# Kernel optimization log

Measured on AMD Instinct MI355X. Metric: run time of the kernel, lower is better.

The kernel has to match this reference:

```python
import jax, jax.numpy as jnp
import numpy as np

D = 768
H = 12
DH = 64
S = 1500
SCALE = 0.125  # 1/sqrt(64)


def setup_inputs() -> dict:
    key = jax.random.key(0)
    ks = jax.random.split(key, 8)
    def w(k):
        return jax.random.normal(k, (D, D), dtype=jnp.float32) * (1.0 / np.sqrt(D))
    x = jax.random.normal(ks[0], (8, S, D), dtype=jnp.float32)
    return {
        "x": x,
        "Wq": w(ks[1]), "bq": jax.random.normal(ks[2], (D,), dtype=jnp.float32) * 0.02,
        "Wk": w(ks[3]),
        "Wv": w(ks[4]), "bv": jax.random.normal(ks[5], (D,), dtype=jnp.float32) * 0.02,
        "Wo": w(ks[6]), "bo": jax.random.normal(ks[7], (D,), dtype=jnp.float32) * 0.02,
    }


def reference(x, Wq, bq, Wk, Wv, bv, Wo, bo):
    B = x.shape[0]
    # torch Linear: y = x @ W.T + b
    q = (jnp.einsum('bsd,ed->bse', x, Wq) + bq) * SCALE
    k = jnp.einsum('bsd,ed->bse', x, Wk)
    v = jnp.einsum('bsd,ed->bse', x, Wv) + bv
    # split heads: [B, S, H, DH] -> [B, H, S, DH]
    q = q.reshape(B, S, H, DH).transpose(0, 2, 1, 3)
    k = k.reshape(B, S, H, DH).transpose(0, 2, 1, 3)
    v = v.reshape(B, S, H, DH).transpose(0, 2, 1, 3)
    scores = jnp.einsum('bhqd,bhkd->bhqk', q, k)  # [B, H, S, S]
    probs = jax.nn.softmax(scores, axis=-1)
    ctx = jnp.einsum('bhqk,bhkd->bhqd', probs, v)
    ctx = ctx.transpose(0, 2, 1, 3).reshape(B, S, D)
    return jnp.einsum('bsd,ed->bse', ctx, Wo) + bo
```

## Files before the change

### kernel.cpp

```cpp
#include <hip/hip_runtime.h>
#include <hip/hip_bf16.h>

constexpr int kD  = 768;
constexpr int kH  = 12;
constexpr int kDH = 64;
constexpr int kS  = 1500;
constexpr int kSP = 1504;
constexpr int kB  = 8;
constexpr int kM  = kB * kS;
constexpr float kScale = 0.125f;
constexpr int kPSTR = 72;
constexpr int kNK = kD / 32;

typedef __bf16 bf16;
typedef __bf16 bf16x4 __attribute__((ext_vector_type(4)));
typedef __bf16 bf16x8 __attribute__((ext_vector_type(8)));
typedef float  floatx4 __attribute__((ext_vector_type(4)));

__global__ __launch_bounds__(256) void detect_kernel(const void* __restrict__ xraw,
                                                     int* __restrict__ flag) {
    __shared__ int bad;
    if (threadIdx.x == 0) bad = 0;
    __syncthreads();
    const bf16* xb = (const bf16*)xraw;
    int c = 0;
    for (int k = 0; k < 16; k++) {
        int idx = 2 * (threadIdx.x + 256 * k);
        float v = fabsf((float)xb[idx]);
        if (!(v == 0.0f || (v > 1e-20f && v < 1e6f))) c++;
    }
    atomicAdd(&bad, c);
    __syncthreads();
    if (threadIdx.x == 0) *flag = (bad > 8) ? 1 : 0;
}

__global__ __launch_bounds__(256) void cvt_bf16_kernel(const void* __restrict__ src,
                                                       bf16* __restrict__ dst, int n,
                                                       const int* __restrict__ flag) {
    int i = blockIdx.x * 256 + threadIdx.x;
    if (i < n) {
        if (*flag)
            dst[i] = (bf16)((const float*)src)[i];
        else
            dst[i] = ((const bf16*)src)[i];
    }
}

__global__ __launch_bounds__(256) void cvt_f32_kernel(const void* __restrict__ src,
                                                      float* __restrict__ dst, int n,
                                                      const int* __restrict__ flag) {
    int i = blockIdx.x * 256 + threadIdx.x;
    if (i < n) {
        if (*flag)
            dst[i] = ((const float*)src)[i];
        else
            dst[i] = (float)((const bf16*)src)[i];
    }
}

__global__ __launch_bounds__(256) void zeropad_kernel(bf16* __restrict__ q_ws,
                                                      bf16* __restrict__ k_ws,
                                                      bf16* __restrict__ vt_ws) {
    int t = blockIdx.x * 256 + threadIdx.x;
    if (t < kB * kH * (kSP - kS) * kDH) {
        int bh  = t >> 8;
        int rem = t & 255;
        int s   = kS + (rem >> 6);
        int dh  = rem & 63;
        size_t qi = ((size_t)bh * kSP + s) * kDH + dh;
        q_ws[qi] = (bf16)0.f;
        k_ws[qi] = (bf16)0.f;
        size_t vi = ((size_t)bh * kDH + dh) * kSP + s;
        vt_ws[vi] = (bf16)0.f;
    }
}

__device__ __forceinline__ void async_copy16(const bf16* g, bf16* l) {
    __builtin_amdgcn_global_load_lds(
        (const __attribute__((address_space(1))) void*)g,
        (__attribute__((address_space(3))) void*)l,
        16, 0, 0);
}

#define G_STAGE(KK, SB)                                                         \
    {                                                                           \
        const int k0_ = (KK) * 32;                                              \
        async_copy16(gA + k0_, Asm + (SB) * 4096 + wof);                        \
        async_copy16(gA + (size_t)64 * kD + k0_, Asm + (SB) * 4096 + wof + 2048); \
        async_copy16(gB + k0_, Bsm + (SB) * 4096 + wof);                        \
        async_copy16(gB + (size_t)64 * kD + k0_, Bsm + (SB) * 4096 + wof + 2048); \
    }

#define G_COMPUTE(CB)                                                           \
    {                                                                           \
        const bf16* A_ = Asm + (CB) * 4096;                                     \
        const bf16* B_ = Bsm + (CB) * 4096;                                     \
        bf16x8 af[4], bfr[4];                                                   \
        _Pragma("unroll") for (int i = 0; i < 4; i++)                           \
            af[i] = *(const bf16x8*)(A_ + ((wm + i * 16 + lrow) << 5) + (lq << 3)); \
        _Pragma("unroll") for (int j = 0; j < 4; j++)                           \
            bfr[j] = *(const bf16x8*)(B_ + ((wn + j * 16 + lrow) << 5) + (lq << 3)); \
        _Pragma("unroll") for (int i = 0; i < 4; i++)                           \
            _Pragma("unroll") for (int j = 0; j < 4; j++)                       \
                acc[i][j] = __builtin_amdgcn_mfma_f32_16x16x32_bf16(            \
                    af[i], bfr[j], acc[i][j], 0, 0, 0);                         \
    }

#define G_STEP(KK, CB, SB)                                                      \
    {                                                                           \
        if ((KK) + 2 < kNK) G_STAGE((KK) + 2, SB);                              \
        G_COMPUTE(CB);                                                          \
        if ((KK) + 1 < kNK) {                                                   \
            if ((KK) + 2 < kNK) {                                               \
                asm volatile("s_waitcnt vmcnt(4)" ::: "memory");                \
            } else {                                                            \
                asm volatile("s_waitcnt vmcnt(0)" ::: "memory");                \
            }                                                                   \
            __builtin_amdgcn_s_barrier();                                       \
            __builtin_amdgcn_sched_barrier(0);                                  \
        }                                                                       \
    }

__device__ __forceinline__ void gemm128_tb(const bf16* __restrict__ X,
                                           const bf16* __restrict__ W,
                                           int m0, int n0,
                                           bf16* Asm, bf16* Bsm,
                                           floatx4 acc[4][4]) {
    const int tid  = threadIdx.x;
    const int lane = tid & 63;
    const int w    = tid >> 6;
    const int srow = (w << 4) + (lane >> 2);
    const int scol = (lane & 3) << 3;
    const int lrow = lane & 15;
    const int lq   = lane >> 4;
    const int wm   = (w >> 1) << 6;
    const int wn   = (w & 1) << 6;

    const bf16* gA = X + (size_t)(m0 + srow) * kD + scol;
    const bf16* gB = W + (size_t)(n0 + srow) * kD + scol;
    const int wof = w << 9;

    G_STAGE(0, 0);
    G_STAGE(1, 1);
    asm volatile("s_waitcnt vmcnt(4)" ::: "memory");
    __builtin_amdgcn_s_barrier();
    __builtin_amdgcn_sched_barrier(0);

#pragma unroll
    for (int ks = 0; ks < kNK; ks += 3) {
        G_STEP(ks,     0, 2);
        G_STEP(ks + 1, 1, 0);
        G_STEP(ks + 2, 2, 1);
    }
}

__global__ __launch_bounds__(256) void qkv_kernel(const bf16* __restrict__ X,
                                                  const bf16* __restrict__ Wq,
                                                  const bf16* __restrict__ Wk,
                                                  const bf16* __restrict__ Wv,
                                                  const float* __restrict__ bq,
                                                  const float* __restrict__ bv,
                                                  bf16* __restrict__ q_ws,
                                                  bf16* __restrict__ k_ws,
                                                  bf16* __restrict__ vt_ws) {
    __shared__ bf16 Asm[3 * 4096];
    __shared__ bf16 Bsm[3 * 4096];

    const int lin = blockIdx.x;
    const int wk  = (lin & 7) * 212 + (lin >> 3);
    if (wk >= 94 * 18) return;
    const int bx  = wk / 18;
    const int r   = wk - bx * 18;
    const int m0  = bx << 7;
    const int mat = r / 6;
    const int n0  = (r % 6) << 7;
    const bf16* W = (mat == 0) ? Wq : (mat == 1) ? Wk : Wv;

    floatx4 acc[4][4] = {};
    gemm128_tb(X, W, m0, n0, Asm, Bsm, acc);

    const int tid  = threadIdx.x;
    const int lane = tid & 63;
    const int w    = tid >> 6;
    const int lrow = lane & 15;
    const int lq   = lane >> 4;
    const int wm   = (w >> 1) << 6;
    const int wn   = (w & 1) << 6;

#pragma unroll
    for (int i = 0; i < 4; i++) {
#pragma unroll
        for (int j = 0; j < 4; j++) {
            const int n  = n0 + wn + j * 16 + lrow;
            const int hh = n >> 6, dh = n & 63;
            const float bval = (mat == 0) ? bq[n] : (mat == 2) ? bv[n] : 0.f;
#pragma unroll
            for (int r2 = 0; r2 < 4; r2++) {
                const int m = m0 + wm + i * 16 + lq * 4 + r2;
                if (m >= kM) continue;
                float v = acc[i][j][r2];
                if (mat == 0)      v = (v + bval) * kScale;
                else if (mat == 2) v = v + bval;
                const int bb = m / kS, s = m - bb * kS;
                if (mat == 2)
                    vt_ws[(((size_t)(bb * kH + hh)) * kDH + dh) * kSP + s] = (bf16)v;
                else if (mat == 1)
                    k_ws[(((size_t)(bb * kH + hh)) * kSP + s) * kDH + dh] = (bf16)v;
                else
                    q_ws[(((size_t)(bb * kH + hh)) * kSP + s) * kDH + dh] = (bf16)v;
            }
        }
    }
}

__global__ __launch_bounds__(256) void out_kernel(const bf16* __restrict__ X,
                                                  const bf16* __restrict__ Wo,
                                                  const float* __restrict__ bo,
                                                  float* __restrict__ outf) {
    __shared__ bf16 Asm[3 * 4096];
    __shared__ bf16 Bsm[3 * 4096];

    const int m0 = blockIdx.x << 7;
    const int n0 = blockIdx.y << 7;

    floatx4 acc[4][4] = {};
    gemm128_tb(X, Wo, m0, n0, Asm, Bsm, acc);

    const int tid  = threadIdx.x;
    const int lane = tid & 63;
    const int w    = tid >> 6;
    const int lrow = lane & 15;
    const int lq   = lane >> 4;
    const int wm   = (w >> 1) << 6;
    const int wn   = (w & 1) << 6;

#pragma unroll
    for (int i = 0; i < 4; i++) {
#pragma unroll
        for (int j = 0; j < 4; j++) {
            const int n = n0 + wn + j * 16 + lrow;
            const float bval = bo[n];
#pragma unroll
            for (int r = 0; r < 4; r++) {
                const int m = m0 + wm + i * 16 + lq * 4 + r;
                if (m >= kM) continue;
                outf[(size_t)m * kD + n] = acc[i][j][r] + bval;
            }
        }
    }
}

__device__ __forceinline__ const bf16* lds_at(const bf16* sm, int row, int cb) {
    return sm + row * 64 + ((cb ^ ((row & 7) << 4)) >> 1);
}

__device__ __forceinline__ void stage_k(const bf16* __restrict__ kbase, int s0,
                                        bf16* ksm, int w, int lane) {
#pragma unroll
    for (int i = 0; i < 2; i++) {
        const int sidx = i * 4 + w;
        const int row  = sidx * 8 + (lane >> 3);
        const int cb   = (lane & 7) << 4;
        const int scb  = cb ^ ((row & 7) << 4);
        int gr = s0 + row;
        if (gr >= kSP) gr = 1472;
        async_copy16(kbase + (size_t)gr * kDH + (scb >> 1), ksm + sidx * 512);
    }
}

__device__ __forceinline__ void stage_v(const bf16* __restrict__ vbase, int s0,
                                        bf16* vsm, int w, int lane) {
#pragma unroll
    for (int i = 0; i < 2; i++) {
        const int sidx = i * 4 + w;
        const int row  = sidx * 8 + (lane >> 3);
        const int cb   = (lane & 7) << 4;
        const int scb  = cb ^ ((row & 7) << 4);
        int key = s0 + (scb >> 1);
        if (key >= kSP) key = 1472;
        async_copy16(vbase + (size_t)row * kSP + key, vsm + sidx * 512);
    }
}

__device__ __forceinline__ void qk_mfma_lds(const bf16* ksm,
                                            const bf16x8 qf[2][2],
                                            floatx4 sc[2][4],
                                            int col, int quad) {
#pragma unroll
    for (int t = 0; t < 4; t++) {
        const int r = 16 * t + col;
        const bf16x8 kf0 = *(const bf16x8*)lds_at(ksm, r, quad * 16);
        const bf16x8 kf1 = *(const bf16x8*)lds_at(ksm, r, 64 + quad * 16);
        __builtin_amdgcn_s_setprio(1);
#pragma unroll
        for (int qt = 0; qt < 2; qt++) {
            floatx4 a = {0.f, 0.f, 0.f, 0.f};
            a = __builtin_amdgcn_mfma_f32_16x16x32_bf16(kf0, qf[qt][0], a, 0, 0, 0);
            a = __builtin_amdgcn_mfma_f32_16x16x32_bf16(kf1, qf[qt][1], a, 0, 0, 0);
            sc[qt][t] = a;
        }
        __builtin_amdgcn_s_setprio(0);
    }
}

template <bool MASK>
__device__ __forceinline__ void exp_store(const floatx4 sc[2][4],
                                          bf16* __restrict__ Pw,
                                          float lsum[2],
                                          int s0, int col, int quad) {
#pragma unroll
    for (int qt = 0; qt < 2; qt++)
#pragma unroll
        for (int t = 0; t < 4; t++) {
            bf16x4 pv;
#pragma unroll
            for (int r = 0; r < 4; r++) {
                float p;
                if (MASK && (s0 + 16 * t + quad * 4 + r >= kS))
                    p = 0.f;
                else
                    p = __expf(sc[qt][t][r]);
                lsum[qt] += p;
                pv[r] = (bf16)p;
            }
            *(bf16x4*)(Pw + (qt * 16 + col) * kPSTR + 16 * t + quad * 4) = pv;
        }
}

__device__ __forceinline__ void pv_lds(const bf16* vsm,
                                       const bf16* __restrict__ Pr,
                                       floatx4 Oacc[2][4],
                                       int col, int quad) {
    bf16x8 pa[2][2];
#pragma unroll
    for (int qt = 0; qt < 2; qt++)
#pragma unroll
        for (int kc = 0; kc < 2; kc++)
            pa[qt][kc] = *(const bf16x8*)(Pr + (qt * 16 + col) * kPSTR + kc * 32 + quad * 8);
#pragma unroll
    for (int n = 0; n < 4; n++) {
        const int row = n * 16 + col;
#pragma unroll
        for (int kc = 0; kc < 2; kc++) {
            const bf16x8 vf = *(const bf16x8*)lds_at(vsm, row, kc * 64 + quad * 16);
            __builtin_amdgcn_s_setprio(1);
#pragma unroll
            for (int qt = 0; qt < 2; qt++)
                Oacc[qt][n] = __builtin_amdgcn_mfma_f32_16x16x32_bf16(
                    pa[qt][kc], vf, Oacc[qt][n], 0, 0, 0);
            __builtin_amdgcn_s_setprio(0);
        }
    }
}

__global__ __launch_bounds__(256, 2) void fattn_kernel(const bf16* __restrict__ q_ws,
                                                       const bf16* __restrict__ k_ws,
                                                       const bf16* __restrict__ vt_ws,
                                                       bf16* __restrict__ ctx) {
    __shared__ bf16 Ksm[2][64 * 64];
    __shared__ bf16 Vsm[2][64 * 64];
    __shared__ bf16 Pbuf[4][32 * kPSTR];

    const int idx = blockIdx.x;
    const int bh  = idx % 96;
    const int qb  = idx / 96;
    const int b   = bh / kH;
    const int h   = bh - b * kH;
    const int tid  = threadIdx.x;
    const int w    = tid >> 6;
    const int lane = tid & 63;
    const int col  = lane & 15;
    const int quad = lane >> 4;
    const int q0   = qb * 128 + w * 32;
    const bool active = (q0 < kS);

    const bf16* qbase = q_ws  + (size_t)bh * kSP * kDH;
    const bf16* kbase = k_ws  + (size_t)bh * kSP * kDH;
    const bf16* vbase = vt_ws + (size_t)bh * kDH * kSP;

    bf16x8 qf[2][2] = {};
    if (active) {
#pragma unroll
        for (int qt = 0; qt < 2; qt++) {
            const bf16* qr = qbase + (size_t)(q0 + qt * 16 + col) * kDH + quad * 8;
            qf[qt][0] = *(const bf16x8*)(qr);
            qf[qt][1] = *(const bf16x8*)(qr + 32);
        }
    }

    float lsum[2] = {0.f, 0.f};
    floatx4 Oacc[2][4];
#pragma unroll
    for (int qt = 0; qt < 2; qt++)
#pragma unroll
        for (int n = 0; n < 4; n++) Oacc[qt][n] = (floatx4){0.f, 0.f, 0.f, 0.f};

    bf16* const P = &Pbuf[w][0];
    floatx4 sc[2][4];

    stage_k(kbase, 0, &Ksm[0][0], w, lane);
    stage_v(vbase, 0, &Vsm[0][0], w, lane);
    __syncthreads();

    int buf = 0;
    for (int c = 0; c < 23; ++c) {
        stage_k(kbase, (c + 1) * 64, &Ksm[buf ^ 1][0], w, lane);
        stage_v(vbase, (c + 1) * 64, &Vsm[buf ^ 1][0], w, lane);
        if (active) {
            qk_mfma_lds(&Ksm[buf][0], qf, sc, col, quad);
            exp_store<false>(sc, P, lsum, c * 64, col, quad);
            pv_lds(&Vsm[buf][0], P, Oacc, col, quad);
        }
        __syncthreads();
        buf ^= 1;
    }
    if (active) {
        qk_mfma_lds(&Ksm[buf][0], qf, sc, col, quad);
        exp_store<true>(sc, P, lsum, 1472, col, quad);
        pv_lds(&Vsm[buf][0], P, Oacc, col, quad);

#pragma unroll
        for (int qt = 0; qt < 2; qt++) {
            float l = lsum[qt];
            l += __shfl_xor(l, 16);
            l += __shfl_xor(l, 32);
            const float rinv_col = 1.0f / l;
            float ri[4];
#pragma unroll
            for (int r = 0; r < 4; r++)
                ri[r] = __shfl(rinv_col, quad * 4 + r, 16);
#pragma unroll
            for (int n = 0; n < 4; n++)
#pragma unroll
                for (int r = 0; r < 4; r++) {
                    const int q = q0 + qt * 16 + quad * 4 + r;
                    if (q < kS)
                        ctx[((size_t)(b * kS + q)) * kD + h * kDH + n * 16 + col] =
                            (bf16)(Oacc[qt][n][r] * ri[r]);
                }
        }
    }
}

extern "C" void kernel_launch(void* const* d_in, const int* in_sizes, int n_in,
                              void* d_out, int out_size, void* d_ws, size_t ws_size,
                              hipStream_t stream) {
    float* out_f = (float*)d_out;

    constexpr size_t nX = (size_t)kM * kD;
    constexpr size_t nW = (size_t)kD * kD;
    constexpr size_t per_qkv = (size_t)kB * kH * kSP * kDH;

    bf16* xb    = (bf16*)d_ws;
    bf16* Wqb   = xb + nX;
    bf16* Wkb   = Wqb + nW;
    bf16* Wvb   = Wkb + nW;
    bf16* Wob   = Wvb + nW;
    bf16* q_ws  = Wob + nW;
    bf16* k_ws  = q_ws + per_qkv;
    bf16* vt_ws = k_ws + per_qkv;
    float* bqf  = (float*)(vt_ws + per_qkv);
    float* bvf  = bqf + kD;
    float* bof  = bvf + kD;
    int*  flag  = (int*)(bof + kD);
    bf16* ctx   = xb;

    detect_kernel<<<1, 256, 0, stream>>>(d_in[0], flag);
    cvt_bf16_kernel<<<(int)((nX + 255) / 256), 256, 0, stream>>>(d_in[0], xb,  (int)nX, flag);
    cvt_bf16_kernel<<<(int)((nW + 255) / 256), 256, 0, stream>>>(d_in[1], Wqb, (int)nW, flag);
    cvt_bf16_kernel<<<(int)((nW + 255) / 256), 256, 0, stream>>>(d_in[3], Wkb, (int)nW, flag);
    cvt_bf16_kernel<<<(int)((nW + 255) / 256), 256, 0, stream>>>(d_in[4], Wvb, (int)nW, flag);
    cvt_bf16_kernel<<<(int)((nW + 255) / 256), 256, 0, stream>>>(d_in[6], Wob, (int)nW, flag);
    cvt_f32_kernel<<<3, 256, 0, stream>>>(d_in[2], bqf, kD, flag);
    cvt_f32_kernel<<<3, 256, 0, stream>>>(d_in[5], bvf, kD, flag);
    cvt_f32_kernel<<<3, 256, 0, stream>>>(d_in[7], bof, kD, flag);

    zeropad_kernel<<<96, 256, 0, stream>>>(q_ws, k_ws, vt_ws);
    qkv_kernel<<<dim3(1696), 256, 0, stream>>>(xb, Wqb, Wkb, Wvb, bqf, bvf,
                                               q_ws, k_ws, vt_ws);

    fattn_kernel<<<dim3(12 * 96), 256, 0, stream>>>(q_ws, k_ws, vt_ws, ctx);

    dim3 ogrid((kM + 127) / 128, kD / 128);
    out_kernel<<<ogrid, 256, 0, stream>>>(ctx, Wob, bof, out_f);
}
```

Measured before the change: 344.7 us.

## Deepen GEMM LDS pipeline to four stages and vectorize V-transpose stores

The shared projection GEMM now keeps three K-tiles in flight instead of two. It uses a 4-buffer LDS ring and adjusted vmcnt waits, so more global-load latency is hidden behind MFMA work. The cost is 64KB of LDS per block instead of 48KB, which can lower how many blocks fit per CU in both the QKV and output kernels. Separately, the V epilogue writes its four consecutive sequence positions as one bf16x4 store into the transposed layout, replacing four scalar strided stores.

```diff
diff --git a/kernel.cpp b/kernel.cpp
--- a/kernel.cpp
+++ b/kernel.cpp
@@ -108,10 +108,12 @@
 
 #define G_STEP(KK, CB, SB)                                                      \
     {                                                                           \
-        if ((KK) + 2 < kNK) G_STAGE((KK) + 2, SB);                              \
+        if ((KK) + 3 < kNK) G_STAGE((KK) + 3, SB);                              \
         G_COMPUTE(CB);                                                          \
         if ((KK) + 1 < kNK) {                                                   \
-            if ((KK) + 2 < kNK) {                                               \
+            if ((KK) + 3 < kNK) {                                               \
+                asm volatile("s_waitcnt vmcnt(8)" ::: "memory");                \
+            } else if ((KK) + 2 < kNK) {                                        \
                 asm volatile("s_waitcnt vmcnt(4)" ::: "memory");                \
             } else {                                                            \
                 asm volatile("s_waitcnt vmcnt(0)" ::: "memory");                \
@@ -121,7 +123,7 @@
         }                                                                       \
     }
 
-__device__ __forceinline__ void gemm128_tb(const bf16* __restrict__ X,
+__device__ __forceinline__ void gemm128_qb(const bf16* __restrict__ X,
                                            const bf16* __restrict__ W,
                                            int m0, int n0,
                                            bf16* Asm, bf16* Bsm,
@@ -142,15 +144,17 @@
 
     G_STAGE(0, 0);
     G_STAGE(1, 1);
-    asm volatile("s_waitcnt vmcnt(4)" ::: "memory");
+    G_STAGE(2, 2);
+    asm volatile("s_waitcnt vmcnt(8)" ::: "memory");
     __builtin_amdgcn_s_barrier();
     __builtin_amdgcn_sched_barrier(0);
 
 #pragma unroll
-    for (int ks = 0; ks < kNK; ks += 3) {
-        G_STEP(ks,     0, 2);
+    for (int ks = 0; ks < kNK; ks += 4) {
+        G_STEP(ks,     0, 3);
         G_STEP(ks + 1, 1, 0);
         G_STEP(ks + 2, 2, 1);
+        G_STEP(ks + 3, 3, 2);
     }
 }
 
@@ -163,8 +167,8 @@
                                                   bf16* __restrict__ q_ws,
                                                   bf16* __restrict__ k_ws,
                                                   bf16* __restrict__ vt_ws) {
-    __shared__ bf16 Asm[3 * 4096];
-    __shared__ bf16 Bsm[3 * 4096];
+    __shared__ bf16 Asm[4 * 4096];
+    __shared__ bf16 Bsm[4 * 4096];
 
     const int lin = blockIdx.x;
     const int wk  = (lin & 7) * 212 + (lin >> 3);
@@ -177,7 +181,7 @@
     const bf16* W = (mat == 0) ? Wq : (mat == 1) ? Wk : Wv;
 
     floatx4 acc[4][4] = {};
-    gemm128_tb(X, W, m0, n0, Asm, Bsm, acc);
+    gemm128_qb(X, W, m0, n0, Asm, Bsm, acc);
 
     const int tid  = threadIdx.x;
     const int lane = tid & 63;
@@ -187,27 +191,41 @@
     const int wm   = (w >> 1) << 6;
     const int wn   = (w & 1) << 6;
 
-#pragma unroll
-    for (int i = 0; i < 4; i++) {
-#pragma unroll
-        for (int j = 0; j < 4; j++) {
-            const int n  = n0 + wn + j * 16 + lrow;
-            const int hh = n >> 6, dh = n & 63;
-            const float bval = (mat == 0) ? bq[n] : (mat == 2) ? bv[n] : 0.f;
-#pragma unroll
-            for (int r2 = 0; r2 < 4; r2++) {
-                const int m = m0 + wm + i * 16 + lq * 4 + r2;
+    if (mat == 2) {
+#pragma unroll
+        for (int i = 0; i < 4; i++) {
+#pragma unroll
+            for (int j = 0; j < 4; j++) {
+                const int n  = n0 + wn + j * 16 + lrow;
+                const int hh = n >> 6, dh = n & 63;
+                const float bval = bv[n];
+                const int m = m0 + wm + i * 16 + lq * 4;
                 if (m >= kM) continue;
-                float v = acc[i][j][r2];
-                if (mat == 0)      v = (v + bval) * kScale;
-                else if (mat == 2) v = v + bval;
                 const int bb = m / kS, s = m - bb * kS;
-                if (mat == 2)
-                    vt_ws[(((size_t)(bb * kH + hh)) * kDH + dh) * kSP + s] = (bf16)v;
-                else if (mat == 1)
-                    k_ws[(((size_t)(bb * kH + hh)) * kSP + s) * kDH + dh] = (bf16)v;
-                else
-                    q_ws[(((size_t)(bb * kH + hh)) * kSP + s) * kDH + dh] = (bf16)v;
+                bf16x4 pv;
+#pragma unroll
+                for (int r2 = 0; r2 < 4; r2++) pv[r2] = (bf16)(acc[i][j][r2] + bval);
+                *(bf16x4*)(vt_ws + (((size_t)(bb * kH + hh)) * kDH + dh) * kSP + s) = pv;
+            }
+        }
+    } else {
+        bf16* const dst = (mat == 0) ? q_ws : k_ws;
+#pragma unroll
+        for (int i = 0; i < 4; i++) {
+#pragma unroll
+            for (int j = 0; j < 4; j++) {
+                const int n  = n0 + wn + j * 16 + lrow;
+                const int hh = n >> 6, dh = n & 63;
+                const float bval = (mat == 0) ? bq[n] : 0.f;
+#pragma unroll
+                for (int r2 = 0; r2 < 4; r2++) {
+                    const int m = m0 + wm + i * 16 + lq * 4 + r2;
+                    if (m >= kM) continue;
+                    float v = acc[i][j][r2];
+                    if (mat == 0) v = (v + bval) * kScale;
+                    const int bb = m / kS, s = m - bb * kS;
+                    dst[(((size_t)(bb * kH + hh)) * kSP + s) * kDH + dh] = (bf16)v;
+                }
             }
         }
     }
@@ -217,14 +235,14 @@
                                                   const bf16* __restrict__ Wo,
                                                   const float* __restrict__ bo,
                                                   float* __restrict__ outf) {
-    __shared__ bf16 Asm[3 * 4096];
-    __shared__ bf16 Bsm[3 * 4096];
+    __shared__ bf16 Asm[4 * 4096];
+    __shared__ bf16 Bsm[4 * 4096];
 
     const int m0 = blockIdx.x << 7;
     const int n0 = blockIdx.y << 7;
 
     floatx4 acc[4][4] = {};
-    gemm128_tb(X, Wo, m0, n0, Asm, Bsm, acc);
+    gemm128_qb(X, Wo, m0, n0, Asm, Bsm, acc);
 
     const int tid  = threadIdx.x;
     const int lane = tid & 63;
```

Measured after the change: 339.1 us. Within noise of the previous version (-1.6%).
